# Kernel optimization log

Measured on AMD Instinct MI355X. Metric: run time of the kernel, lower is better.

Reference implementation:

```python
import jax, jax.numpy as jnp
import numpy as np

NUM_ITERS = 3


def squash(s):
    # s: [..., V]
    sq = (s ** 2).sum(-1, keepdims=True)
    return sq * s / ((1.0 + sq) * jnp.sqrt(sq))


def setup_inputs() -> dict:
    key = jax.random.key(0)
    kx, kw = jax.random.split(key)
    B, O, I, V, D = 32, 1, 4096, 512, 8
    x = jax.random.normal(kx, (B, I, D), dtype=jnp.float32)
    W = 0.01 * jax.random.normal(kw, (O, I, V, D), dtype=jnp.float32)
    return {"x": x, "W": W}


def reference(x, W):
    B = x.shape[0]
    O, I, V, _ = W.shape
    # x_hat[b,o,i,v] = sum_d W[o,i,v,d] * x[b,i,d]
    x_hat = jnp.einsum('oivd,bid->boiv', W, x)  # [B,O,I,V]
    x_hat_d = jax.lax.stop_gradient(x_hat)

    b = jnp.zeros((B, O, I), dtype=x.dtype)
    for it in range(NUM_ITERS):
        c = jax.nn.softmax(b, axis=1)  # over out caps
        if it == NUM_ITERS - 1:
            outputs = squash((c[:, :, :, None] * x_hat).sum(-2, keepdims=True))
        else:
            outputs = squash((c[:, :, :, None] * x_hat_d).sum(-2, keepdims=True))
            b = b + (outputs * x_hat_d).sum(-1)

    outputs = outputs.squeeze(-2)  # [B,O,V]
    # decode_idx == -1 branch
    classes = jax.nn.softmax(jnp.sqrt((outputs ** 2).sum(2)), axis=1)  # [B,O]
    max_idx = jnp.argmax(classes, axis=1)  # [B]
    masked = jax.nn.one_hot(max_idx, O, dtype=outputs.dtype)  # [B,O]
    t = (outputs * masked[:, :, None]).sum(axis=1)[:, None, :]  # [B,1,V]
    return (t, outputs)
```

## Files before the change

### kernel.cpp

```cpp
#include <hip/hip_runtime.h>
#include <stdint.h>


#define NB 32
#define NI 4096
#define NV 512
#define ND 8
#define NK 32768
#define KB 64
#define KSB (NK / KB)
#define KSW 32

typedef __fp16 f16x8 __attribute__((ext_vector_type(8)));
typedef __fp16 f16x4 __attribute__((ext_vector_type(4)));
typedef __fp16 f16x2 __attribute__((ext_vector_type(2)));
typedef float  f32x16 __attribute__((ext_vector_type(16)));

__global__ __launch_bounds__(1024) void caps_mfma(
    const float* __restrict__ W, const float* __restrict__ x,
    __fp16* __restrict__ partial_h)
{
    const int t    = threadIdx.x;
    const int lane = t & 63;
    const int wave = t >> 6;
    const int half = lane >> 5;
    const int ln32 = lane & 31;

    const int kb = blockIdx.x & (KB - 1);
    const int vg = blockIdx.x >> 6;
    const int v0 = vg * 32;

    const int g0l = wave * 4 + half;
    const int g1l = g0l + 2;
    const int g0  = kb * (KSB / 8) + g0l;
    const int g1  = g0 + 2;

    const float4* wp0 = (const float4*)(W + ((size_t)g0 * NV + v0 + ln32) * ND);
    const float4* wp1 = (const float4*)(W + ((size_t)g1 * NV + v0 + ln32) * ND);
    const float4 w00 = wp0[0];
    const float4 w01 = wp0[1];
    const float4 w10 = wp1[0];
    const float4 w11 = wp1[1];

    __shared__ __align__(16) __fp16 xs[2 * 16384];

    const int r = t >> 5;
    const int c = t & 31;
    const float* xrow = x + (size_t)r * NK + (size_t)kb * KSB;
#pragma unroll
    for (int j = 0; j < 4; ++j) {
        const int kl = (c + 32 * j) * 4;
        const float4 f = *(const float4*)(xrow + kl);
        const int gp   = kl >> 3;
        const int part = (kl >> 2) & 1;
        const f16x2 hA = __builtin_amdgcn_cvt_pkrtz(f.x, f.y);
        const f16x2 hB = __builtin_amdgcn_cvt_pkrtz(f.z, f.w);
        const f16x2 lA = __builtin_amdgcn_cvt_pkrtz(f.x - (float)hA.x, f.y - (float)hA.y);
        const f16x2 lB = __builtin_amdgcn_cvt_pkrtz(f.z - (float)hB.x, f.w - (float)hB.y);
        const int eoff = gp * 256 + ((r * 8 + part * 4) ^ ((gp & 7) << 3));
        *(f16x4*)(xs + eoff)         = (f16x4){hA.x, hA.y, hB.x, hB.y};
        *(f16x4*)(xs + 16384 + eoff) = (f16x4){lA.x, lA.y, lB.x, lB.y};
    }
    __syncthreads();

    const int e0 = g0l * 256 + ((ln32 * 8) ^ ((g0l & 7) << 3));
    const int e1 = g1l * 256 + ((ln32 * 8) ^ ((g1l & 7) << 3));
    const f16x8 a0h = *(const f16x8*)(xs + e0);
    const f16x8 a0l = *(const f16x8*)(xs + 16384 + e0);
    const f16x8 a1h = *(const f16x8*)(xs + e1);
    const f16x8 a1l = *(const f16x8*)(xs + 16384 + e1);

    const f16x2 p01 = __builtin_amdgcn_cvt_pkrtz(w00.x, w00.y);
    const f16x2 p23 = __builtin_amdgcn_cvt_pkrtz(w00.z, w00.w);
    const f16x2 p45 = __builtin_amdgcn_cvt_pkrtz(w01.x, w01.y);
    const f16x2 p67 = __builtin_amdgcn_cvt_pkrtz(w01.z, w01.w);
    const f16x8 b0 = {p01.x, p01.y, p23.x, p23.y, p45.x, p45.y, p67.x, p67.y};
    const f16x2 q01 = __builtin_amdgcn_cvt_pkrtz(w10.x, w10.y);
    const f16x2 q23 = __builtin_amdgcn_cvt_pkrtz(w10.z, w10.w);
    const f16x2 q45 = __builtin_amdgcn_cvt_pkrtz(w11.x, w11.y);
    const f16x2 q67 = __builtin_amdgcn_cvt_pkrtz(w11.z, w11.w);
    const f16x8 b1 = {q01.x, q01.y, q23.x, q23.y, q45.x, q45.y, q67.x, q67.y};

    f32x16 acc;
#pragma unroll
    for (int rr = 0; rr < 16; ++rr) acc[rr] = 0.0f;
    acc = __builtin_amdgcn_mfma_f32_32x32x16_f16(a0h, b0, acc, 0, 0, 0);
    acc = __builtin_amdgcn_mfma_f32_32x32x16_f16(a0l, b0, acc, 0, 0, 0);
    acc = __builtin_amdgcn_mfma_f32_32x32x16_f16(a1h, b1, acc, 0, 0, 0);
    acc = __builtin_amdgcn_mfma_f32_32x32x16_f16(a1l, b1, acc, 0, 0, 0);

    __syncthreads();
    float* red = (float*)xs;
#pragma unroll
    for (int rr = 0; rr < 16; ++rr)
        red[wave * 1024 + rr * 64 + lane] = acc[rr];
    __syncthreads();

    float val = 0.0f;
#pragma unroll
    for (int w = 0; w < 16; ++w)
        val += red[w * 1024 + t];

    const int rg = t >> 6;
    const int ln = t & 63;
    const int row = (rg & 3) + 8 * (rg >> 2) + 4 * (ln >> 5);
    const int col = ln & 31;
    partial_h[((size_t)kb * NB + row) * NV + v0 + col] = (__fp16)val;
}

__global__ __launch_bounds__(1024) void caps_finish(
    const __fp16* __restrict__ partial_h, float* __restrict__ out)
{
    const int t = threadIdx.x;
    const int v = t & 511;
    const int h = t >> 9;
    const int b = blockIdx.x;

    float s = 0.0f;
#pragma unroll
    for (int g = 0; g < KB / 2; ++g)
        s += (float)partial_h[((size_t)(h * (KB / 2) + g) * NB + b) * NV + v];

    __shared__ float sv[1024];
    sv[t] = s;
    __syncthreads();

    float sq = 0.0f;
    float stot = 0.0f;
    if (t < 512) {
        stot = sv[t] + sv[t + 512];
        sq = stot * stot;
    }
#pragma unroll
    for (int off = 32; off > 0; off >>= 1)
        sq += __shfl_xor(sq, off, 64);

    __shared__ float red[16];
    if ((t & 63) == 0) red[t >> 6] = sq;
    __syncthreads();
    if (t < 512) {
        float tot = 0.0f;
#pragma unroll
        for (int wv = 0; wv < 16; ++wv) tot += red[wv];

        const float factor = sqrtf(tot) / (1.0f + tot);
        const float r = stot * factor;

        out[(size_t)b * NV + v]           = r;
        out[NB * NV + (size_t)b * NV + v] = r;
    }
}

extern "C" void kernel_launch(void* const* d_in, const int* in_sizes, int n_in,
                              void* d_out, int out_size, void* d_ws, size_t ws_size,
                              hipStream_t stream) {
    const float* x = (const float*)d_in[0];
    const float* W = (const float*)d_in[1];
    float* out     = (float*)d_out;

    __fp16* partialh = (__fp16*)d_ws;

    caps_mfma<<<KB * 16, 1024, 0, stream>>>(W, x, partialh);
    caps_finish<<<NB, 1024, 0, stream>>>(partialh, out);
}
```

Before: 100.6 us.

## Process two K-chunks per block to halve split-K partials

Each block now loops over two K sub-chunks, accumulating both into the same MFMA accumulator, so the split-K factor drops from 64 to 32. This halves the partial-sum writes, the cross-wave LDS reductions and the finish-kernel reads. The second W tile is loaded after the first MFMAs, which may reduce the number of memory requests in flight. The grid also halves, which lowers parallelism.

```diff
diff --git a/kernel.cpp b/kernel.cpp
--- a/kernel.cpp
+++ b/kernel.cpp
@@ -7,9 +7,8 @@
 #define NV 512
 #define ND 8
 #define NK 32768
-#define KB 64
+#define KB 32
 #define KSB (NK / KB)
-#define KSW 32
 
 typedef __fp16 f16x8 __attribute__((ext_vector_type(8)));
 typedef __fp16 f16x4 __attribute__((ext_vector_type(4)));
@@ -27,69 +26,84 @@
     const int ln32 = lane & 31;
 
     const int kb = blockIdx.x & (KB - 1);
-    const int vg = blockIdx.x >> 6;
+    const int vg = blockIdx.x >> 5;
     const int v0 = vg * 32;
 
     const int g0l = wave * 4 + half;
     const int g1l = g0l + 2;
-    const int g0  = kb * (KSB / 8) + g0l;
-    const int g1  = g0 + 2;
 
-    const float4* wp0 = (const float4*)(W + ((size_t)g0 * NV + v0 + ln32) * ND);
-    const float4* wp1 = (const float4*)(W + ((size_t)g1 * NV + v0 + ln32) * ND);
-    const float4 w00 = wp0[0];
-    const float4 w01 = wp0[1];
-    const float4 w10 = wp1[0];
-    const float4 w11 = wp1[1];
+    const int e0 = g0l * 256 + ((ln32 * 8) ^ ((g0l & 7) << 3));
+    const int e1 = g1l * 256 + ((ln32 * 8) ^ ((g1l & 7) << 3));
 
     __shared__ __align__(16) __fp16 xs[2 * 16384];
 
     const int r = t >> 5;
     const int c = t & 31;
-    const float* xrow = x + (size_t)r * NK + (size_t)kb * KSB;
-#pragma unroll
-    for (int j = 0; j < 4; ++j) {
-        const int kl = (c + 32 * j) * 4;
-        const float4 f = *(const float4*)(xrow + kl);
-        const int gp   = kl >> 3;
-        const int part = (kl >> 2) & 1;
-        const f16x2 hA = __builtin_amdgcn_cvt_pkrtz(f.x, f.y);
-        const f16x2 hB = __builtin_amdgcn_cvt_pkrtz(f.z, f.w);
-        const f16x2 lA = __builtin_amdgcn_cvt_pkrtz(f.x - (float)hA.x, f.y - (float)hA.y);
-        const f16x2 lB = __builtin_amdgcn_cvt_pkrtz(f.z - (float)hB.x, f.w - (float)hB.y);
-        const int eoff = gp * 256 + ((r * 8 + part * 4) ^ ((gp & 7) << 3));
-        *(f16x4*)(xs + eoff)         = (f16x4){hA.x, hA.y, hB.x, hB.y};
-        *(f16x4*)(xs + 16384 + eoff) = (f16x4){lA.x, lA.y, lB.x, lB.y};
-    }
-    __syncthreads();
-
-    const int e0 = g0l * 256 + ((ln32 * 8) ^ ((g0l & 7) << 3));
-    const int e1 = g1l * 256 + ((ln32 * 8) ^ ((g1l & 7) << 3));
-    const f16x8 a0h = *(const f16x8*)(xs + e0);
-    const f16x8 a0l = *(const f16x8*)(xs + 16384 + e0);
-    const f16x8 a1h = *(const f16x8*)(xs + e1);
-    const f16x8 a1l = *(const f16x8*)(xs + 16384 + e1);
-
-    const f16x2 p01 = __builtin_amdgcn_cvt_pkrtz(w00.x, w00.y);
-    const f16x2 p23 = __builtin_amdgcn_cvt_pkrtz(w00.z, w00.w);
-    const f16x2 p45 = __builtin_amdgcn_cvt_pkrtz(w01.x, w01.y);
-    const f16x2 p67 = __builtin_amdgcn_cvt_pkrtz(w01.z, w01.w);
-    const f16x8 b0 = {p01.x, p01.y, p23.x, p23.y, p45.x, p45.y, p67.x, p67.y};
-    const f16x2 q01 = __builtin_amdgcn_cvt_pkrtz(w10.x, w10.y);
-    const f16x2 q23 = __builtin_amdgcn_cvt_pkrtz(w10.z, w10.w);
-    const f16x2 q45 = __builtin_amdgcn_cvt_pkrtz(w11.x, w11.y);
-    const f16x2 q67 = __builtin_amdgcn_cvt_pkrtz(w11.z, w11.w);
-    const f16x8 b1 = {q01.x, q01.y, q23.x, q23.y, q45.x, q45.y, q67.x, q67.y};
 
     f32x16 acc;
 #pragma unroll
     for (int rr = 0; rr < 16; ++rr) acc[rr] = 0.0f;
-    acc = __builtin_amdgcn_mfma_f32_32x32x16_f16(a0h, b0, acc, 0, 0, 0);
-    acc = __builtin_amdgcn_mfma_f32_32x32x16_f16(a0l, b0, acc, 0, 0, 0);
-    acc = __builtin_amdgcn_mfma_f32_32x32x16_f16(a1h, b1, acc, 0, 0, 0);
-    acc = __builtin_amdgcn_mfma_f32_32x32x16_f16(a1l, b1, acc, 0, 0, 0);
 
-    __syncthreads();
+    const int gW0 = kb * (KSB / 8) + g0l;
+    const float4* wq0 = (const float4*)(W + ((size_t)gW0 * NV + v0 + ln32) * ND);
+    const float4* wq1 = (const float4*)(W + ((size_t)(gW0 + 2) * NV + v0 + ln32) * ND);
+    float4 w00 = wq0[0];
+    float4 w01 = wq0[1];
+    float4 w10 = wq1[0];
+    float4 w11 = wq1[1];
+
+#pragma unroll
+    for (int p = 0; p < 2; ++p) {
+        const float* xrow = x + (size_t)r * NK + (size_t)kb * KSB + p * 512;
+#pragma unroll
+        for (int j = 0; j < 4; ++j) {
+            const int kl = (c + 32 * j) * 4;
+            const float4 f = *(const float4*)(xrow + kl);
+            const int gp   = kl >> 3;
+            const int part = (kl >> 2) & 1;
+            const f16x2 hA = __builtin_amdgcn_cvt_pkrtz(f.x, f.y);
+            const f16x2 hB = __builtin_amdgcn_cvt_pkrtz(f.z, f.w);
+            const f16x2 lA = __builtin_amdgcn_cvt_pkrtz(f.x - (float)hA.x, f.y - (float)hA.y);
+            const f16x2 lB = __builtin_amdgcn_cvt_pkrtz(f.z - (float)hB.x, f.w - (float)hB.y);
+            const int eoff = gp * 256 + ((r * 8 + part * 4) ^ ((gp & 7) << 3));
+            *(f16x4*)(xs + eoff)         = (f16x4){hA.x, hA.y, hB.x, hB.y};
+            *(f16x4*)(xs + 16384 + eoff) = (f16x4){lA.x, lA.y, lB.x, lB.y};
+        }
+        __syncthreads();
+
+        const f16x8 a0h = *(const f16x8*)(xs + e0);
+        const f16x8 a0l = *(const f16x8*)(xs + 16384 + e0);
+        const f16x8 a1h = *(const f16x8*)(xs + e1);
+        const f16x8 a1l = *(const f16x8*)(xs + 16384 + e1);
+
+        const f16x2 p01 = __builtin_amdgcn_cvt_pkrtz(w00.x, w00.y);
+        const f16x2 p23 = __builtin_amdgcn_cvt_pkrtz(w00.z, w00.w);
+        const f16x2 p45 = __builtin_amdgcn_cvt_pkrtz(w01.x, w01.y);
+        const f16x2 p67 = __builtin_amdgcn_cvt_pkrtz(w01.z, w01.w);
+        const f16x8 b0 = {p01.x, p01.y, p23.x, p23.y, p45.x, p45.y, p67.x, p67.y};
+        const f16x2 q01 = __builtin_amdgcn_cvt_pkrtz(w10.x, w10.y);
+        const f16x2 q23 = __builtin_amdgcn_cvt_pkrtz(w10.z, w10.w);
+        const f16x2 q45 = __builtin_amdgcn_cvt_pkrtz(w11.x, w11.y);
+        const f16x2 q67 = __builtin_amdgcn_cvt_pkrtz(w11.z, w11.w);
+        const f16x8 b1 = {q01.x, q01.y, q23.x, q23.y, q45.x, q45.y, q67.x, q67.y};
+
+        acc = __builtin_amdgcn_mfma_f32_32x32x16_f16(a0h, b0, acc, 0, 0, 0);
+        acc = __builtin_amdgcn_mfma_f32_32x32x16_f16(a0l, b0, acc, 0, 0, 0);
+        acc = __builtin_amdgcn_mfma_f32_32x32x16_f16(a1h, b1, acc, 0, 0, 0);
+        acc = __builtin_amdgcn_mfma_f32_32x32x16_f16(a1l, b1, acc, 0, 0, 0);
+
+        if (p == 0) {
+            const int gW1 = gW0 + 64;
+            const float4* wr0 = (const float4*)(W + ((size_t)gW1 * NV + v0 + ln32) * ND);
+            const float4* wr1 = (const float4*)(W + ((size_t)(gW1 + 2) * NV + v0 + ln32) * ND);
+            w00 = wr0[0];
+            w01 = wr0[1];
+            w10 = wr1[0];
+            w11 = wr1[1];
+        }
+        __syncthreads();
+    }
+
     float* red = (float*)xs;
 #pragma unroll
     for (int rr = 0; rr < 16; ++rr)
```

Result: no change. 100.9 us (+0.3%).
